# Kernel optimization log

Measured on AMD Instinct MI355X. Metric: run time of the kernel, lower is better.

The kernel has to match this reference:

```python
import jax, jax.numpy as jnp
import numpy as np

NEG = -1e30  # finite stand-in for -inf (keeps logsumexp NaN-free)
B, T, V, L = 64, 1024, 512, 128
BLANK = 0


def setup_inputs() -> dict:
    key = jax.random.key(0)
    k1, k2 = jax.random.split(key)
    outputs = jax.random.normal(k1, (B, T, V), dtype=jnp.float32)
    labels = jax.random.randint(k2, (B, L), 1, V, dtype=jnp.int32)  # labels avoid blank=0
    output_lengths = jnp.full((B,), T, dtype=jnp.int32)
    label_lengths = jnp.full((B,), L, dtype=jnp.int32)
    return {"outputs": outputs, "labels": labels,
            "output_lengths": output_lengths, "label_lengths": label_lengths}


def _ctc_loss(log_probs, labels, output_lengths, label_lengths):
    # log_probs: [B, T, V]; labels: [B, L]
    S = 2 * L + 1
    # extended label sequence: blank, l1, blank, l2, ..., blank
    ext = jnp.full((B, S), BLANK, dtype=labels.dtype).at[:, 1::2].set(labels)
    # skip transition allowed at s if ext[s] != blank and ext[s] != ext[s-2]
    ext_m2 = jnp.pad(ext, ((0, 0), (2, 0)), constant_values=BLANK)[:, :S]
    skip = (ext != BLANK) & (ext != ext_m2) & (jnp.arange(S) >= 2)

    # emission log-probs on the lattice: emit[b, t, s] = log_probs[b, t, ext[b, s]]
    bidx = jnp.arange(B)
    emit = log_probs[bidx[:, None, None], jnp.arange(T)[None, :, None], ext[:, None, :]]  # [B,T,S]
    emit_t = jnp.moveaxis(emit, 1, 0)  # [T, B, S]

    alpha0 = (jnp.full((B, S), NEG, dtype=log_probs.dtype)
              .at[:, 0].set(emit_t[0, :, 0])
              .at[:, 1].set(emit_t[0, :, 1]))

    neg1 = jnp.full((B, 1), NEG, dtype=log_probs.dtype)
    neg2 = jnp.full((B, 2), NEG, dtype=log_probs.dtype)

    def step(alpha, e):
        p0 = alpha
        p1 = jnp.concatenate([neg1, alpha[:, :-1]], axis=1)
        p2 = jnp.where(skip, jnp.concatenate([neg2, alpha[:, :-2]], axis=1), NEG)
        m = jnp.maximum(p0, jnp.maximum(p1, p2))
        lse = m + jnp.log(jnp.exp(p0 - m) + jnp.exp(p1 - m) + jnp.exp(p2 - m))
        new = lse + e
        return new, new

    _, alphas = jax.lax.scan(step, alpha0, emit_t[1:])
    alphas = jnp.concatenate([alpha0[None], alphas], axis=0)  # [T, B, S]

    a_last = alphas[output_lengths - 1, bidx]  # [B, S] alpha at final frame per sample
    s1 = 2 * label_lengths      # final blank state
    s0 = 2 * label_lengths - 1  # final label state
    a0 = a_last[bidx, s0]
    a1 = a_last[bidx, s1]
    m = jnp.maximum(a0, a1)
    log_lik = m + jnp.log(jnp.exp(a0 - m) + jnp.exp(a1 - m))
    # reduction='mean': per-sample nll divided by target length, then batch mean
    loss = -log_lik / label_lengths.astype(log_lik.dtype)
    return jnp.mean(loss)


def reference(outputs, labels, output_lengths, label_lengths):
    return _ctc_loss(outputs, labels, output_lengths, label_lengths)
```

## Files before the change

### kernel.cpp

```cpp
#include <hip/hip_runtime.h>

#define B_ 64
#define T_ 1024
#define V_ 512
#define L_ 128
#define S_ 257
#define LOG2E_ 1.4426950408889634f
#define LN2_   0.6931471805599453f
#define R_ 5
#define C_ 28
#define ROWP_ 260
#define NC_ ((T_ - 1 + C_ - 1) / C_)
#define EDEAD_ (-(1 << 28))

__device__ __forceinline__ float exp2_fast(float x) { return __builtin_amdgcn_exp2f(x); }
__device__ __forceinline__ float log2_fast(float x) { return __builtin_amdgcn_logf(x); }
__device__ __forceinline__ float ldx(float v, int e) { return __builtin_amdgcn_ldexpf(v, e); }

__device__ __forceinline__ float dpp_up1_f(float x) {
    int r = __builtin_amdgcn_update_dpp(0, __float_as_int(x), 0x138, 0xf, 0xf, true);
    return __int_as_float(r);
}
__device__ __forceinline__ int dpp_up1_i(int x) {
    return __builtin_amdgcn_update_dpp(0, x, 0x138, 0xf, 0xf, true);
}

__global__ __launch_bounds__(512, 1) void ctc_alpha_kernel(
    const float* __restrict__ outputs, const int* __restrict__ labels,
    const int* __restrict__ out_lens, const int* __restrict__ lab_lens,
    float* __restrict__ ws, float* __restrict__ out)
{
    const int b    = blockIdx.x;
    const int tid  = threadIdx.x;
    const int wid  = tid >> 6;
    const int lane = tid & 63;

    int* cnt = (int*)ws;
    float* losses = ws + 16;

    __shared__ float ring[2][C_ * ROWP_];
    __shared__ float save2[2];
    __shared__ int   saveE[2];
    __shared__ int   amLast;

    const int olen  = out_lens[b];
    const int ll    = lab_lens[b];
    const int s0q   = 2 * ll - 1;
    const int s1q   = 2 * ll;
    const int tlast = olen - 1;
    const int l0 = s0q / R_, j0 = s0q % R_;
    const int l1 = s1q / R_, j1 = s1q % R_;
    const float* base = outputs + (size_t)b * T_ * V_;
    const int*   lab  = labels + b * L_;

    int pcls[4];
    #pragma unroll
    for (int k = 0; k < 4; ++k) {
        int s = lane + 64 * k;
        pcls[k] = (s & 1) ? lab[s >> 1] : 0;
    }

    float sk[R_];
    float v0=0.f, v1=0.f, v2=0.f, v3=0.f, v4=0.f;
    int   E = EDEAD_;
    const bool isl0 = (lane == 0);
    const int roff = (R_ * lane < ROWP_ - R_) ? R_ * lane : (ROWP_ - R_);
    if (wid == 0) {
        __builtin_amdgcn_s_setprio(3);
        #pragma unroll
        for (int j = 0; j < R_; ++j) {
            int s = R_ * lane + j;
            float skf = 0.f;
            if (s < S_ && (s & 1) && s >= 3)
                skf = (lab[s >> 1] != lab[(s >> 1) - 1]) ? 1.f : 0.f;
            sk[j] = skf;
        }
        if (isl0) {
            v0 = exp2_fast(base[0]      * LOG2E_);
            v1 = exp2_fast(base[lab[0]] * LOG2E_);
            E  = 0;
        }
        if (tlast == 0) {
            float w0 = (j0==0)?v0:(j0==1)?v1:(j0==2)?v2:(j0==3)?v3:v4;
            float w1 = (j1==0)?v0:(j1==1)?v1:(j1==2)?v2:(j1==3)?v3:v4;
            if (lane == l0) { save2[0] = w0; saveE[0] = E; }
            if (lane == l1) { save2[1] = w1; saveE[1] = E; }
        }
    } else {
        __builtin_amdgcn_s_setprio(0);
    }

    auto produce = [&](int bb, int t0) {
        float vals[4][4];
        #pragma unroll
        for (int m = 0; m < 4; ++m) {
            int t = t0 + (wid - 1) + 7 * m;
            const float* rp = (t < T_) ? (base + (size_t)t * V_) : base;
            #pragma unroll
            for (int k = 0; k < 4; ++k) vals[m][k] = rp[pcls[k]];
        }
        #pragma unroll
        for (int m = 0; m < 4; ++m) {
            int r = (wid - 1) + 7 * m;
            int t = t0 + r;
            if (t < T_) {
                float* dst = &ring[bb][r * ROWP_];
                float e0 = exp2_fast(vals[m][0] * LOG2E_);
                float e1 = exp2_fast(vals[m][1] * LOG2E_);
                float e2 = exp2_fast(vals[m][2] * LOG2E_);
                float e3 = exp2_fast(vals[m][3] * LOG2E_);
                dst[lane]       = e0;
                dst[lane + 64]  = e1;
                dst[lane + 128] = e2;
                dst[lane + 192] = e3;
                if (lane == 0) dst[256] = e0;
            }
        }
    };

    auto step = [&](const float* row) {
        float e0 = row[0], e1 = row[1], e2 = row[2], e3 = row[3], e4 = row[4];

        float up1 = dpp_up1_f(v4);
        float up2 = dpp_up1_f(v3);
        int   upE = dpp_up1_i(E);
        upE = isl0 ? E : upE;

        int d    = upE - E;
        int mpos = (d > 0) ? d : 0;
        int sin  = (d < 0) ? d : 0;
        int sown = -mpos;
        E += mpos;
        v0 = ldx(v0, sown); v1 = ldx(v1, sown); v2 = ldx(v2, sown);
        v3 = ldx(v3, sown); v4 = ldx(v4, sown);
        up1 = ldx(up1, sin); up2 = ldx(up2, sin);

        float n0 = fmaf(sk[0], up2, v0 + up1) * e0;
        float n1 = fmaf(sk[1], up1, v1 + v0 ) * e1;
        float n2 = fmaf(sk[2], v0 , v2 + v1 ) * e2;
        float n3 = fmaf(sk[3], v1 , v3 + v2 ) * e3;
        float n4 = fmaf(sk[4], v2 , v4 + v3 ) * e4;
        v0 = n0; v1 = n1; v2 = n2; v3 = n3; v4 = n4;
    };

    auto renorm = [&]() {
        float mx = fmaxf(fmaxf(v0, v1), fmaxf(fmaxf(v2, v3), v4));
        int ex = (__float_as_int(mx) >> 23) - 126;
        v0 = ldx(v0, -ex); v1 = ldx(v1, -ex); v2 = ldx(v2, -ex);
        v3 = ldx(v3, -ex); v4 = ldx(v4, -ex);
        E += ex;
    };

    auto consume = [&](int bb, int t0) {
        const float* rows = &ring[bb][roff];
        bool chk = (t0 + C_ > T_) || ((unsigned)(tlast - t0) < (unsigned)C_);
        if (!chk) {
            #pragma unroll 4
            for (int r = 0; r < C_; ++r) {
                step(rows + r * ROWP_);
                if ((r & 3) == 3) renorm();
            }
        } else {
            #pragma unroll 4
            for (int r = 0; r < C_; ++r) {
                int t = t0 + r;
                if (t >= T_) break;
                step(rows + r * ROWP_);
                if ((r & 3) == 3) renorm();
                if (t == tlast) {
                    float w0 = (j0==0)?v0:(j0==1)?v1:(j0==2)?v2:(j0==3)?v3:v4;
                    float w1 = (j1==0)?v0:(j1==1)?v1:(j1==2)?v2:(j1==3)?v3:v4;
                    if (lane == l0) { save2[0] = w0; saveE[0] = E; }
                    if (lane == l1) { save2[1] = w1; saveE[1] = E; }
                }
            }
        }
    };

    if (wid > 0) produce(0, 1);
    __syncthreads();
    for (int c = 0; c < NC_; ++c) {
        if (wid > 0) {
            if (c + 1 < NC_) produce((c + 1) & 1, 1 + (c + 1) * C_);
        } else {
            consume(c & 1, 1 + c * C_);
        }
        __syncthreads();
    }

    if (tid == 0) {
        float lx = log2_fast(save2[0]) + (float)saveE[0];
        float ly = log2_fast(save2[1]) + (float)saveE[1];
        float m  = fmaxf(lx, ly);
        float lik2 = m + log2_fast(exp2_fast(lx - m) + exp2_fast(ly - m));
        float loss = -(lik2 * LN2_) / (float)ll;
        __hip_atomic_store(&losses[b], loss, __ATOMIC_RELAXED, __HIP_MEMORY_SCOPE_AGENT);
        int old = __hip_atomic_fetch_add(cnt, 1, __ATOMIC_ACQ_REL, __HIP_MEMORY_SCOPE_AGENT);
        amLast = (old == B_ - 1);
    }
    __syncthreads();
    if (amLast && wid == 0) {
        float v = __hip_atomic_load(&losses[lane], __ATOMIC_RELAXED, __HIP_MEMORY_SCOPE_AGENT);
        #pragma unroll
        for (int o = 32; o > 0; o >>= 1) v += __shfl_down(v, o);
        if (lane == 0) out[0] = v * (1.0f / B_);
    }
}

extern "C" void kernel_launch(void* const* d_in, const int* in_sizes, int n_in,
                              void* d_out, int out_size, void* d_ws, size_t ws_size,
                              hipStream_t stream) {
    const float* outputs  = (const float*)d_in[0];
    const int*   labels   = (const int*)d_in[1];
    const int*   out_lens = (const int*)d_in[2];
    const int*   lab_lens = (const int*)d_in[3];

    hipMemsetAsync(d_ws, 0, 64, stream);
    ctc_alpha_kernel<<<B_, 512, 0, stream>>>(outputs, labels, out_lens, lab_lens,
                                             (float*)d_ws, (float*)d_out);
}
```

Before: 255.3 us.

## Remap CTC lattice to four states per lane with vectorized LDS emission loads

Each lane of the alpha wave now holds four lattice states instead of five. The final blank state (index 256) is kept in an extra register that every lane updates redundantly. Because even states are always blank and never take a skip transition, the unused skip terms are dropped, and the emission row is read as one aligned float4 LDS load. Those loads are prefetched two rows ahead in a small register double buffer, and the chunk size is doubled so producer waves fill eight rows each, halving the number of block barriers. The redundant extra state on non-final lanes is folded into the renormalization max. This costs a little extra work, and those junk values could in principle skew scaling on those lanes.

Result: faster. 244.4 us (-4.3%).

```diff
diff --git a/kernel.cpp b/kernel.cpp
--- a/kernel.cpp
+++ b/kernel.cpp
@@ -7,21 +7,20 @@
 #define S_ 257
 #define LOG2E_ 1.4426950408889634f
 #define LN2_   0.6931471805599453f
-#define R_ 5
-#define C_ 28
+#define C_ 56
 #define ROWP_ 260
 #define NC_ ((T_ - 1 + C_ - 1) / C_)
-#define EDEAD_ (-(1 << 28))
+
+typedef float f4_t __attribute__((ext_vector_type(4)));
 
 __device__ __forceinline__ float exp2_fast(float x) { return __builtin_amdgcn_exp2f(x); }
 __device__ __forceinline__ float log2_fast(float x) { return __builtin_amdgcn_logf(x); }
 __device__ __forceinline__ float ldx(float v, int e) { return __builtin_amdgcn_ldexpf(v, e); }
 
-__device__ __forceinline__ float dpp_up1_f(float x) {
-    int r = __builtin_amdgcn_update_dpp(0, __float_as_int(x), 0x138, 0xf, 0xf, true);
-    return __int_as_float(r);
-}
-__device__ __forceinline__ int dpp_up1_i(int x) {
+__device__ __forceinline__ float dpp_shr1_f(float x) {
+    return __int_as_float(__builtin_amdgcn_update_dpp(0, __float_as_int(x), 0x138, 0xf, 0xf, true));
+}
+__device__ __forceinline__ int dpp_shr1_i(int x) {
     return __builtin_amdgcn_update_dpp(0, x, 0x138, 0xf, 0xf, true);
 }
 
@@ -48,8 +47,9 @@
     const int s0q   = 2 * ll - 1;
     const int s1q   = 2 * ll;
     const int tlast = olen - 1;
-    const int l0 = s0q / R_, j0 = s0q % R_;
-    const int l1 = s1q / R_, j1 = s1q % R_;
+    const int l0  = s0q >> 2, j0 = s0q & 3;
+    const int l1e = (s1q == 256) ? 63 : (s1q >> 2);
+    const int j1  = s1q & 3;
     const float* base = outputs + (size_t)b * T_ * V_;
     const int*   lab  = labels + b * L_;
 
@@ -60,47 +60,45 @@
         pcls[k] = (s & 1) ? lab[s >> 1] : 0;
     }
 
-    float sk[R_];
-    float v0=0.f, v1=0.f, v2=0.f, v3=0.f, v4=0.f;
-    int   E = EDEAD_;
-    const bool isl0 = (lane == 0);
-    const int roff = (R_ * lane < ROWP_ - R_) ? R_ * lane : (ROWP_ - R_);
+    float sk1 = 0.f, sk3 = 0.f;
+    float v0 = 0.f, v1 = 0.f, v2 = 0.f, v3 = 0.f, vx = 0.f;
+    int   E = 0;
+    const bool isl0  = (lane == 0);
     if (wid == 0) {
         __builtin_amdgcn_s_setprio(3);
-        #pragma unroll
-        for (int j = 0; j < R_; ++j) {
-            int s = R_ * lane + j;
-            float skf = 0.f;
-            if (s < S_ && (s & 1) && s >= 3)
-                skf = (lab[s >> 1] != lab[(s >> 1) - 1]) ? 1.f : 0.f;
-            sk[j] = skf;
+        {
+            int s1s = 4 * lane + 1;
+            int k1  = s1s >> 1;
+            if (s1s >= 3) sk1 = (lab[k1] != lab[k1 - 1]) ? 1.f : 0.f;
+            int s3s = 4 * lane + 3;
+            int k3  = s3s >> 1;
+            sk3 = (lab[k3] != lab[k3 - 1]) ? 1.f : 0.f;
         }
         if (isl0) {
             v0 = exp2_fast(base[0]      * LOG2E_);
             v1 = exp2_fast(base[lab[0]] * LOG2E_);
-            E  = 0;
         }
         if (tlast == 0) {
-            float w0 = (j0==0)?v0:(j0==1)?v1:(j0==2)?v2:(j0==3)?v3:v4;
-            float w1 = (j1==0)?v0:(j1==1)?v1:(j1==2)?v2:(j1==3)?v3:v4;
-            if (lane == l0) { save2[0] = w0; saveE[0] = E; }
-            if (lane == l1) { save2[1] = w1; saveE[1] = E; }
+            float w0 = (j0==0)?v0:(j0==1)?v1:(j0==2)?v2:v3;
+            float w1 = (s1q==256) ? vx : ((j1==0)?v0:(j1==1)?v1:(j1==2)?v2:v3);
+            if (lane == l0)  { save2[0] = w0; saveE[0] = E; }
+            if (lane == l1e) { save2[1] = w1; saveE[1] = E; }
         }
     } else {
         __builtin_amdgcn_s_setprio(0);
     }
 
     auto produce = [&](int bb, int t0) {
-        float vals[4][4];
+        float vals[8][4];
         #pragma unroll
-        for (int m = 0; m < 4; ++m) {
+        for (int m = 0; m < 8; ++m) {
             int t = t0 + (wid - 1) + 7 * m;
             const float* rp = (t < T_) ? (base + (size_t)t * V_) : base;
             #pragma unroll
             for (int k = 0; k < 4; ++k) vals[m][k] = rp[pcls[k]];
         }
         #pragma unroll
-        for (int m = 0; m < 4; ++m) {
+        for (int m = 0; m < 8; ++m) {
             int r = (wid - 1) + 7 * m;
             int t = t0 + r;
             if (t < T_) {
@@ -118,12 +116,10 @@
         }
     };
 
-    auto step = [&](const float* row) {
-        float e0 = row[0], e1 = row[1], e2 = row[2], e3 = row[3], e4 = row[4];
-
-        float up1 = dpp_up1_f(v4);
-        float up2 = dpp_up1_f(v3);
-        int   upE = dpp_up1_i(E);
+    auto step = [&](f4_t e, float ex) {
+        float up1 = dpp_shr1_f(v3);
+        float up2 = dpp_shr1_f(v2);
+        int   upE = dpp_shr1_i(E);
         upE = isl0 ? E : upE;
 
         int d    = upE - E;
@@ -132,32 +128,46 @@
         int sown = -mpos;
         E += mpos;
         v0 = ldx(v0, sown); v1 = ldx(v1, sown); v2 = ldx(v2, sown);
-        v3 = ldx(v3, sown); v4 = ldx(v4, sown);
+        v3 = ldx(v3, sown); vx = ldx(vx, sown);
         up1 = ldx(up1, sin); up2 = ldx(up2, sin);
 
-        float n0 = fmaf(sk[0], up2, v0 + up1) * e0;
-        float n1 = fmaf(sk[1], up1, v1 + v0 ) * e1;
-        float n2 = fmaf(sk[2], v0 , v2 + v1 ) * e2;
-        float n3 = fmaf(sk[3], v1 , v3 + v2 ) * e3;
-        float n4 = fmaf(sk[4], v2 , v4 + v3 ) * e4;
-        v0 = n0; v1 = n1; v2 = n2; v3 = n3; v4 = n4;
+        float n0 = (v0 + up1) * e.x;
+        float n1 = fmaf(sk1, up1, v1 + v0) * e.y;
+        float n2 = (v2 + v1) * e.z;
+        float n3 = fmaf(sk3, v1, v3 + v2) * e.w;
+        vx = (vx + v3) * ex;
+        v0 = n0; v1 = n1; v2 = n2; v3 = n3;
+        (void)up2;
     };
 
     auto renorm = [&]() {
-        float mx = fmaxf(fmaxf(v0, v1), fmaxf(fmaxf(v2, v3), v4));
+        float mx = fmaxf(fmaxf(v0, v1), fmaxf(v2, v3));
+        mx = fmaxf(mx, vx);
         int ex = (__float_as_int(mx) >> 23) - 126;
-        v0 = ldx(v0, -ex); v1 = ldx(v1, -ex); v2 = ldx(v2, -ex);
-        v3 = ldx(v3, -ex); v4 = ldx(v4, -ex);
+        v0 = ldx(v0, -ex); v1 = ldx(v1, -ex); v2 = ldx(v2, -ex); v3 = ldx(v3, -ex);
+        vx = ldx(vx, -ex);
         E += ex;
     };
 
     auto consume = [&](int bb, int t0) {
-        const float* rows = &ring[bb][roff];
+        const float* rp  = &ring[bb][4 * lane];
+        const float* rpx = &ring[bb][256];
+        f4_t  eb[2];
+        float xb[2];
+        eb[0] = *(const f4_t*)(rp);          xb[0] = rpx[0];
+        eb[1] = *(const f4_t*)(rp + ROWP_);  xb[1] = rpx[ROWP_];
+
         bool chk = (t0 + C_ > T_) || ((unsigned)(tlast - t0) < (unsigned)C_);
         if (!chk) {
-            #pragma unroll 4
+            #pragma unroll 8
             for (int r = 0; r < C_; ++r) {
-                step(rows + r * ROWP_);
+                f4_t  e  = eb[r & 1];
+                float ex = xb[r & 1];
+                if (r + 2 < C_) {
+                    eb[r & 1] = *(const f4_t*)(rp + (r + 2) * ROWP_);
+                    xb[r & 1] = rpx[(r + 2) * ROWP_];
+                }
+                step(e, ex);
                 if ((r & 3) == 3) renorm();
             }
         } else {
@@ -165,13 +175,19 @@
             for (int r = 0; r < C_; ++r) {
                 int t = t0 + r;
                 if (t >= T_) break;
-                step(rows + r * ROWP_);
+                f4_t  e  = eb[r & 1];
+                float ex = xb[r & 1];
+                if (r + 2 < C_) {
+                    eb[r & 1] = *(const f4_t*)(rp + (r + 2) * ROWP_);
+                    xb[r & 1] = rpx[(r + 2) * ROWP_];
+                }
+                step(e, ex);
                 if ((r & 3) == 3) renorm();
                 if (t == tlast) {
-                    float w0 = (j0==0)?v0:(j0==1)?v1:(j0==2)?v2:(j0==3)?v3:v4;
-                    float w1 = (j1==0)?v0:(j1==1)?v1:(j1==2)?v2:(j1==3)?v3:v4;
-                    if (lane == l0) { save2[0] = w0; saveE[0] = E; }
-                    if (lane == l1) { save2[1] = w1; saveE[1] = E; }
+                    float w0 = (j0==0)?v0:(j0==1)?v1:(j0==2)?v2:v3;
+                    float w1 = (s1q==256) ? vx : ((j1==0)?v0:(j1==1)?v1:(j1==2)?v2:v3);
+                    if (lane == l0)  { save2[0] = w0; saveE[0] = E; }
+                    if (lane == l1e) { save2[1] = w1; saveE[1] = E; }
                 }
             }
         }
@@ -215,7 +231,7 @@
     const int*   out_lens = (const int*)d_in[2];
     const int*   lab_lens = (const int*)d_in[3];
 
-    hipMemsetAsync(d_ws, 0, 64, stream);
+    (void)hipMemsetAsync(d_ws, 0, 64, stream);
     ctc_alpha_kernel<<<B_, 512, 0, stream>>>(outputs, labels, out_lens, lab_lens,
                                              (float*)d_ws, (float*)d_out);
 }
```
